# Optimization experiments

Measured on AMD Instinct MI355X. Metric: run time of the kernel, lower is better.

Reference implementation:

```python
import jax, jax.numpy as jnp
import numpy as np

C = 1.0                      # ball curvature c
SQRT_C = 1.0                 # sqrt(c)
EPS = 1e-15                  # norm clamp
BALL_EPS = 1e-5              # projection margin
B, DIN, DOUT = 262144, 128, 128


def artanh(u):
    u = jnp.clip(u, -1.0 + 1e-7, 1.0 - 1e-7)
    return 0.5 * (jnp.log1p(u) - jnp.log1p(-u))


def mobius_matvec(W, x):
    # x: [B, din], W: [dout, din]
    x_norm = jnp.clip(jnp.linalg.norm(x, axis=-1, keepdims=True), EPS)
    Mx = x @ W.T                                   # [B, dout]
    Mx_norm = jnp.clip(jnp.linalg.norm(Mx, axis=-1, keepdims=True), EPS)
    scale = jnp.tanh(Mx_norm / x_norm * artanh(SQRT_C * x_norm)) / (Mx_norm * SQRT_C)
    res = scale * Mx
    return jnp.where(Mx_norm <= 1e-10, 0.0, res)


def mobius_add(x, y):
    # x: [B, d], y broadcastable to [B, d]
    x2 = jnp.sum(x * x, axis=-1, keepdims=True)
    y2 = jnp.sum(y * y, axis=-1, keepdims=True)
    xy = jnp.sum(x * y, axis=-1, keepdims=True)
    num = (1.0 + 2.0 * C * xy + C * y2) * x + (1.0 - C * x2) * y
    den = jnp.clip(1.0 + 2.0 * C * xy + C * C * x2 * y2, EPS)
    return num / den


def projx(x):
    norm = jnp.clip(jnp.linalg.norm(x, axis=-1, keepdims=True), EPS)
    maxnorm = (1.0 - BALL_EPS) / SQRT_C
    return jnp.where(norm > maxnorm, x / norm * maxnorm, x)


def setup_inputs() -> dict:
    key = jax.random.key(0)
    k1, k2, k3 = jax.random.split(key, 3)
    # points strictly inside the unit ball: randn * 0.05 -> norm ~ 0.57 max tail-safe
    x = jax.random.normal(k1, (B, DIN), dtype=jnp.float32) * 0.05
    fan = np.sqrt(6.0 / (DIN + DOUT))  # xavier_uniform scale
    weight = jax.random.uniform(k2, (DOUT, DIN), dtype=jnp.float32, minval=-fan, maxval=fan)
    bias = jax.random.normal(k3, (DOUT,), dtype=jnp.float32) * 0.05
    return {"x": x, "weight": weight, "bias": bias}


def reference(x, weight, bias):
    y = mobius_matvec(weight, x)
    y = mobius_add(y, bias[None, :])
    return projx(y)
```

## Files before the change

kernel.cpp:

```cpp
#include <hip/hip_runtime.h>

typedef __attribute__((ext_vector_type(8))) short short8;
typedef __attribute__((ext_vector_type(4))) float floatx4;

__device__ __forceinline__ unsigned short f2b(float f) {
    union { float f; unsigned int i; } v; v.f = f;
    unsigned int u = v.i;
    u += 0x7FFFu + ((u >> 16) & 1u);
    return (unsigned short)(u >> 16);
}

__global__ __launch_bounds__(256) void mobius_linear_kernel(
    const float* __restrict__ X,
    const float* __restrict__ W,
    const float* __restrict__ Bias,
    float* __restrict__ Out)
{
    __shared__ unsigned short ldsW[128 * 136];

    const int tid  = threadIdx.x;
    const int wave = tid >> 6;
    const int lane = tid & 63;
    const int q = lane >> 4;
    const int c = lane & 15;

#pragma unroll
    for (int i = 0; i < 8; ++i) {
        int chunk = i * 256 + tid;
        int row = chunk >> 4, cc = chunk & 15;
        const float* src = W + row * 128 + cc * 8;
        floatx4 w0 = *reinterpret_cast<const floatx4*>(src);
        floatx4 w1 = *reinterpret_cast<const floatx4*>(src + 4);
        short8 pk;
#pragma unroll
        for (int j = 0; j < 4; ++j) { pk[j] = (short)f2b(w0[j]); pk[4 + j] = (short)f2b(w1[j]); }
        *reinterpret_cast<short8*>(&ldsW[row * 136 + cc * 8]) = pk;
    }

    float bias_f[8];
#pragma unroll
    for (int n = 0; n < 8; ++n) bias_f[n] = Bias[n * 16 + c];
    float b2 = 0.f;
#pragma unroll
    for (int n = 0; n < 8; ++n) b2 = fmaf(bias_f[n], bias_f[n], b2);
    b2 += __shfl_xor(b2, 1);
    b2 += __shfl_xor(b2, 2);
    b2 += __shfl_xor(b2, 4);
    b2 += __shfl_xor(b2, 8);

    const int rowbase = blockIdx.x * 128 + wave * 32;

    short8 afrag[2][4];
    float xn2[2] = {0.f, 0.f};
#pragma unroll
    for (int g = 0; g < 2; ++g) {
        const float* xrow = X + (size_t)(rowbase + g * 16 + c) * 128;
#pragma unroll
        for (int kc = 0; kc < 4; ++kc) {
            const float* src = xrow + kc * 32 + q * 8;
            floatx4 x0 = *reinterpret_cast<const floatx4*>(src);
            floatx4 x1 = *reinterpret_cast<const floatx4*>(src + 4);
            short8 pk;
#pragma unroll
            for (int j = 0; j < 4; ++j) {
                xn2[g] = fmaf(x0[j], x0[j], xn2[g]);
                xn2[g] = fmaf(x1[j], x1[j], xn2[g]);
                pk[j] = (short)f2b(x0[j]); pk[4 + j] = (short)f2b(x1[j]);
            }
            afrag[g][kc] = pk;
        }
    }
    xn2[0] += __shfl_xor(xn2[0], 16); xn2[0] += __shfl_xor(xn2[0], 32);
    xn2[1] += __shfl_xor(xn2[1], 16); xn2[1] += __shfl_xor(xn2[1], 32);

    __syncthreads();

    floatx4 acc[2][8];
#pragma unroll
    for (int g = 0; g < 2; ++g)
#pragma unroll
        for (int n = 0; n < 8; ++n)
            acc[g][n] = (floatx4){0.f, 0.f, 0.f, 0.f};

#pragma unroll
    for (int kc = 0; kc < 4; ++kc) {
#pragma unroll
        for (int n = 0; n < 8; ++n) {
            short8 bf = *reinterpret_cast<const short8*>(
                &ldsW[(n * 16 + c) * 136 + kc * 32 + q * 8]);
            acc[0][n] = __builtin_amdgcn_mfma_f32_16x16x32_bf16(afrag[0][kc], bf, acc[0][n], 0, 0, 0);
            acc[1][n] = __builtin_amdgcn_mfma_f32_16x16x32_bf16(afrag[1][kc], bf, acc[1][n], 0, 0, 0);
        }
    }

#pragma unroll
    for (int g = 0; g < 2; ++g) {
        float m2[4], mb[4];
#pragma unroll
        for (int r = 0; r < 4; ++r) {
            float s2 = 0.f, sb = 0.f;
#pragma unroll
            for (int n = 0; n < 8; ++n) {
                float v = acc[g][n][r];
                s2 = fmaf(v, v, s2);
                sb = fmaf(v, bias_f[n], sb);
            }
            m2[r] = s2; mb[r] = sb;
        }
#pragma unroll
        for (int r = 0; r < 4; ++r) {
            m2[r] += __shfl_xor(m2[r], 1); mb[r] += __shfl_xor(mb[r], 1);
            m2[r] += __shfl_xor(m2[r], 2); mb[r] += __shfl_xor(mb[r], 2);
            m2[r] += __shfl_xor(m2[r], 4); mb[r] += __shfl_xor(mb[r], 4);
            m2[r] += __shfl_xor(m2[r], 8); mb[r] += __shfl_xor(mb[r], 8);
        }
#pragma unroll
        for (int r = 0; r < 4; ++r) {
            float xr2   = __shfl(xn2[g], q * 4 + r);
            float xnorm = fmaxf(sqrtf(xr2), 1e-15f);
            float u     = fminf(xnorm, 1.f - 1e-7f);
            float at    = 0.5f * __logf((1.f + u) / (1.f - u));
            float Mxn   = fmaxf(sqrtf(m2[r]), 1e-15f);
            float arg   = Mxn / xnorm * at;
            float e     = __expf(2.f * arg);
            float th    = 1.f - 2.f / (e + 1.f);
            float scale = (Mxn <= 1e-10f) ? 0.f : th / Mxn;
            float y2 = scale * scale * m2[r];
            float yb = scale * mb[r];
            float t1  = 1.f + 2.f * yb + b2;
            float den = fmaxf(fmaf(y2, b2, 1.f + 2.f * yb), 1e-15f);
            float Af = t1 * scale / den;
            float Bf = (1.f - y2) / den;
            float zn2 = Af * Af * m2[r] + 2.f * Af * Bf * mb[r] + Bf * Bf * b2;
            float zn  = fmaxf(sqrtf(zn2), 1e-15f);
            const float maxn = 1.f - 1e-5f;
            float fac = (zn > maxn) ? (maxn / zn) : 1.f;
            Af *= fac; Bf *= fac;

            int row = rowbase + g * 16 + q * 4 + r;
            float* orow = Out + (size_t)row * 128;
#pragma unroll
            for (int n = 0; n < 8; ++n) {
                orow[n * 16 + c] = fmaf(Af, acc[g][n][r], Bf * bias_f[n]);
            }
        }
    }
}

extern "C" void kernel_launch(void* const* d_in, const int* in_sizes, int n_in,
                              void* d_out, int out_size, void* d_ws, size_t ws_size,
                              hipStream_t stream) {
    const float* X    = (const float*)d_in[0];
    const float* W    = (const float*)d_in[1];
    const float* Bias = (const float*)d_in[2];
    float* Out = (float*)d_out;

    dim3 grid(2048), block(256);
    hipLaunchKernelGGL(mobius_linear_kernel, grid, block, 0, stream, X, W, Bias, Out);
}
```

Baseline: 251.8 us.

## Pre-convert weights to bf16 in a separate kernel and drop LDS staging

Adds a small kernel that converts W to bf16 once into the workspace. The main kernel then reads B fragments straight from global memory (cached) instead of having every block convert W and stage it in LDS. It also halves rows per wave (16 instead of 32) and doubles the grid to 4096 blocks, adding a launch-bounds occupancy hint. This removes the per-block W conversion, the LDS traffic and the __syncthreads, at the cost of an extra launch, repeated global or L2 weight reads per wave, and less reuse of each weight fragment.

```diff
diff --git a/kernel.cpp b/kernel.cpp
--- a/kernel.cpp
+++ b/kernel.cpp
@@ -1,6 +1,7 @@
 #include <hip/hip_runtime.h>
 
 typedef __attribute__((ext_vector_type(8))) short short8;
+typedef __attribute__((ext_vector_type(4))) short short4v;
 typedef __attribute__((ext_vector_type(4))) float floatx4;
 
 __device__ __forceinline__ unsigned short f2b(float f) {
@@ -10,32 +11,30 @@
     return (unsigned short)(u >> 16);
 }
 
-__global__ __launch_bounds__(256) void mobius_linear_kernel(
+__global__ __launch_bounds__(256) void convert_w_kernel(
+    const float* __restrict__ W, unsigned short* __restrict__ Wb)
+{
+    int i = (blockIdx.x * 256 + threadIdx.x) * 4;
+    floatx4 w = *reinterpret_cast<const floatx4*>(W + i);
+    short4v p;
+#pragma unroll
+    for (int j = 0; j < 4; ++j) p[j] = (short)f2b(w[j]);
+    *reinterpret_cast<short4v*>(Wb + i) = p;
+}
+
+__global__ __launch_bounds__(256, 5) void mobius_linear_kernel(
     const float* __restrict__ X,
-    const float* __restrict__ W,
+    const unsigned short* __restrict__ Wb,
     const float* __restrict__ Bias,
     float* __restrict__ Out)
 {
-    __shared__ unsigned short ldsW[128 * 136];
-
     const int tid  = threadIdx.x;
     const int wave = tid >> 6;
     const int lane = tid & 63;
     const int q = lane >> 4;
     const int c = lane & 15;
 
-#pragma unroll
-    for (int i = 0; i < 8; ++i) {
-        int chunk = i * 256 + tid;
-        int row = chunk >> 4, cc = chunk & 15;
-        const float* src = W + row * 128 + cc * 8;
-        floatx4 w0 = *reinterpret_cast<const floatx4*>(src);
-        floatx4 w1 = *reinterpret_cast<const floatx4*>(src + 4);
-        short8 pk;
-#pragma unroll
-        for (int j = 0; j < 4; ++j) { pk[j] = (short)f2b(w0[j]); pk[4 + j] = (short)f2b(w1[j]); }
-        *reinterpret_cast<short8*>(&ldsW[row * 136 + cc * 8]) = pk;
-    }
+    const int rowbase = blockIdx.x * 64 + wave * 16;
 
     float bias_f[8];
 #pragma unroll
@@ -48,101 +47,87 @@
     b2 += __shfl_xor(b2, 4);
     b2 += __shfl_xor(b2, 8);
 
-    const int rowbase = blockIdx.x * 128 + wave * 32;
+    short8 afrag[4];
+    float xn2 = 0.f;
+    const float* xrow = X + (size_t)(rowbase + c) * 128;
+#pragma unroll
+    for (int kc = 0; kc < 4; ++kc) {
+        const float* src = xrow + kc * 32 + q * 8;
+        floatx4 x0 = *reinterpret_cast<const floatx4*>(src);
+        floatx4 x1 = *reinterpret_cast<const floatx4*>(src + 4);
+        short8 pk;
+#pragma unroll
+        for (int j = 0; j < 4; ++j) {
+            xn2 = fmaf(x0[j], x0[j], xn2);
+            xn2 = fmaf(x1[j], x1[j], xn2);
+            pk[j] = (short)f2b(x0[j]); pk[4 + j] = (short)f2b(x1[j]);
+        }
+        afrag[kc] = pk;
+    }
+    xn2 += __shfl_xor(xn2, 16);
+    xn2 += __shfl_xor(xn2, 32);
 
-    short8 afrag[2][4];
-    float xn2[2] = {0.f, 0.f};
+    floatx4 acc[8];
 #pragma unroll
-    for (int g = 0; g < 2; ++g) {
-        const float* xrow = X + (size_t)(rowbase + g * 16 + c) * 128;
+    for (int n = 0; n < 8; ++n) acc[n] = (floatx4){0.f, 0.f, 0.f, 0.f};
+
+#pragma unroll
+    for (int n = 0; n < 8; ++n) {
+        const unsigned short* wrow = Wb + (n * 16 + c) * 128 + q * 8;
 #pragma unroll
         for (int kc = 0; kc < 4; ++kc) {
-            const float* src = xrow + kc * 32 + q * 8;
-            floatx4 x0 = *reinterpret_cast<const floatx4*>(src);
-            floatx4 x1 = *reinterpret_cast<const floatx4*>(src + 4);
-            short8 pk;
-#pragma unroll
-            for (int j = 0; j < 4; ++j) {
-                xn2[g] = fmaf(x0[j], x0[j], xn2[g]);
-                xn2[g] = fmaf(x1[j], x1[j], xn2[g]);
-                pk[j] = (short)f2b(x0[j]); pk[4 + j] = (short)f2b(x1[j]);
-            }
-            afrag[g][kc] = pk;
-        }
-    }
-    xn2[0] += __shfl_xor(xn2[0], 16); xn2[0] += __shfl_xor(xn2[0], 32);
-    xn2[1] += __shfl_xor(xn2[1], 16); xn2[1] += __shfl_xor(xn2[1], 32);
-
-    __syncthreads();
-
-    floatx4 acc[2][8];
-#pragma unroll
-    for (int g = 0; g < 2; ++g)
-#pragma unroll
-        for (int n = 0; n < 8; ++n)
-            acc[g][n] = (floatx4){0.f, 0.f, 0.f, 0.f};
-
-#pragma unroll
-    for (int kc = 0; kc < 4; ++kc) {
-#pragma unroll
-        for (int n = 0; n < 8; ++n) {
-            short8 bf = *reinterpret_cast<const short8*>(
-                &ldsW[(n * 16 + c) * 136 + kc * 32 + q * 8]);
-            acc[0][n] = __builtin_amdgcn_mfma_f32_16x16x32_bf16(afrag[0][kc], bf, acc[0][n], 0, 0, 0);
-            acc[1][n] = __builtin_amdgcn_mfma_f32_16x16x32_bf16(afrag[1][kc], bf, acc[1][n], 0, 0, 0);
+            short8 bf = *reinterpret_cast<const short8*>(wrow + kc * 32);
+            acc[n] = __builtin_amdgcn_mfma_f32_16x16x32_bf16(afrag[kc], bf, acc[n], 0, 0, 0);
         }
     }
 
+    float m2[4], mb[4];
 #pragma unroll
-    for (int g = 0; g < 2; ++g) {
-        float m2[4], mb[4];
+    for (int r = 0; r < 4; ++r) {
+        float s2 = 0.f, sb = 0.f;
 #pragma unroll
-        for (int r = 0; r < 4; ++r) {
-            float s2 = 0.f, sb = 0.f;
+        for (int n = 0; n < 8; ++n) {
+            float v = acc[n][r];
+            s2 = fmaf(v, v, s2);
+            sb = fmaf(v, bias_f[n], sb);
+        }
+        m2[r] = s2; mb[r] = sb;
+    }
 #pragma unroll
-            for (int n = 0; n < 8; ++n) {
-                float v = acc[g][n][r];
-                s2 = fmaf(v, v, s2);
-                sb = fmaf(v, bias_f[n], sb);
-            }
-            m2[r] = s2; mb[r] = sb;
-        }
+    for (int r = 0; r < 4; ++r) {
+        m2[r] += __shfl_xor(m2[r], 1); mb[r] += __shfl_xor(mb[r], 1);
+        m2[r] += __shfl_xor(m2[r], 2); mb[r] += __shfl_xor(mb[r], 2);
+        m2[r] += __shfl_xor(m2[r], 4); mb[r] += __shfl_xor(mb[r], 4);
+        m2[r] += __shfl_xor(m2[r], 8); mb[r] += __shfl_xor(mb[r], 8);
+    }
 #pragma unroll
-        for (int r = 0; r < 4; ++r) {
-            m2[r] += __shfl_xor(m2[r], 1); mb[r] += __shfl_xor(mb[r], 1);
-            m2[r] += __shfl_xor(m2[r], 2); mb[r] += __shfl_xor(mb[r], 2);
-            m2[r] += __shfl_xor(m2[r], 4); mb[r] += __shfl_xor(mb[r], 4);
-            m2[r] += __shfl_xor(m2[r], 8); mb[r] += __shfl_xor(mb[r], 8);
-        }
+    for (int r = 0; r < 4; ++r) {
+        float xr2   = __shfl(xn2, q * 4 + r);
+        float xnorm = fmaxf(sqrtf(xr2), 1e-15f);
+        float u     = fminf(xnorm, 1.f - 1e-7f);
+        float at    = 0.5f * __logf((1.f + u) / (1.f - u));
+        float Mxn   = fmaxf(sqrtf(m2[r]), 1e-15f);
+        float arg   = Mxn / xnorm * at;
+        float e     = __expf(2.f * arg);
+        float th    = 1.f - 2.f / (e + 1.f);
+        float scale = (Mxn <= 1e-10f) ? 0.f : th / Mxn;
+        float y2 = scale * scale * m2[r];
+        float yb = scale * mb[r];
+        float t1  = 1.f + 2.f * yb + b2;
+        float den = fmaxf(fmaf(y2, b2, 1.f + 2.f * yb), 1e-15f);
+        float Af = t1 * scale / den;
+        float Bf = (1.f - y2) / den;
+        float zn2 = Af * Af * m2[r] + 2.f * Af * Bf * mb[r] + Bf * Bf * b2;
+        float zn  = fmaxf(sqrtf(zn2), 1e-15f);
+        const float maxn = 1.f - 1e-5f;
+        float fac = (zn > maxn) ? (maxn / zn) : 1.f;
+        Af *= fac; Bf *= fac;
+
+        int row = rowbase + q * 4 + r;
+        float* orow = Out + (size_t)row * 128;
 #pragma unroll
-        for (int r = 0; r < 4; ++r) {
-            float xr2   = __shfl(xn2[g], q * 4 + r);
-            float xnorm = fmaxf(sqrtf(xr2), 1e-15f);
-            float u     = fminf(xnorm, 1.f - 1e-7f);
-            float at    = 0.5f * __logf((1.f + u) / (1.f - u));
-            float Mxn   = fmaxf(sqrtf(m2[r]), 1e-15f);
-            float arg   = Mxn / xnorm * at;
-            float e     = __expf(2.f * arg);
-            float th    = 1.f - 2.f / (e + 1.f);
-            float scale = (Mxn <= 1e-10f) ? 0.f : th / Mxn;
-            float y2 = scale * scale * m2[r];
-            float yb = scale * mb[r];
-            float t1  = 1.f + 2.f * yb + b2;
-            float den = fmaxf(fmaf(y2, b2, 1.f + 2.f * yb), 1e-15f);
-            float Af = t1 * scale / den;
-            float Bf = (1.f - y2) / den;
-            float zn2 = Af * Af * m2[r] + 2.f * Af * Bf * mb[r] + Bf * Bf * b2;
-            float zn  = fmaxf(sqrtf(zn2), 1e-15f);
-            const float maxn = 1.f - 1e-5f;
-            float fac = (zn > maxn) ? (maxn / zn) : 1.f;
-            Af *= fac; Bf *= fac;
-
-            int row = rowbase + g * 16 + q * 4 + r;
-            float* orow = Out + (size_t)row * 128;
-#pragma unroll
-            for (int n = 0; n < 8; ++n) {
-                orow[n * 16 + c] = fmaf(Af, acc[g][n][r], Bf * bias_f[n]);
-            }
+        for (int n = 0; n < 8; ++n) {
+            orow[n * 16 + c] = fmaf(Af, acc[n][r], Bf * bias_f[n]);
         }
     }
 }
@@ -154,7 +139,9 @@
     const float* W    = (const float*)d_in[1];
     const float* Bias = (const float*)d_in[2];
     float* Out = (float*)d_out;
+    unsigned short* Wb = (unsigned short*)d_ws;
 
-    dim3 grid(2048), block(256);
-    hipLaunchKernelGGL(mobius_linear_kernel, grid, block, 0, stream, X, W, Bias, Out);
+    hipLaunchKernelGGL(convert_w_kernel, dim3(16), dim3(256), 0, stream, W, Wb);
+    hipLaunchKernelGGL(mobius_linear_kernel, dim3(4096), dim3(256), 0, stream,
+                       X, Wb, Bias, Out);
 }
```

After: 277.3 us. +10.1%, slower.

## Pre-convert weights to bf16, swizzle LDS, permute output columns for vector stores

Applied to the files above, without the earlier changes.

Adds a small pre-kernel that converts W to bf16 once into workspace, so each block loads half the bytes and skips per-block conversion. The LDS layout is changed from padded to XOR-style swizzled. The N-column mapping is permuted so each lane owns 8 contiguous output columns, which allows 16-byte vector stores and vector bias loads instead of scalar strided stores. X packing now uses a perm-based bf16 truncation with rounding, and launch bounds request 4 waves per SIMD. The cost is an extra kernel launch.

```diff
diff --git a/kernel.cpp b/kernel.cpp
--- a/kernel.cpp
+++ b/kernel.cpp
@@ -1,6 +1,8 @@
 #include <hip/hip_runtime.h>
 
 typedef __attribute__((ext_vector_type(8))) short short8;
+typedef __attribute__((ext_vector_type(4))) short short4v;
+typedef __attribute__((ext_vector_type(4))) int   int4v;
 typedef __attribute__((ext_vector_type(4))) float floatx4;
 
 __device__ __forceinline__ unsigned short f2b(float f) {
@@ -10,13 +12,30 @@
     return (unsigned short)(u >> 16);
 }
 
-__global__ __launch_bounds__(256) void mobius_linear_kernel(
+__device__ __forceinline__ int pack2(float f0, float f1) {
+    unsigned int u0 = __float_as_uint(f0) + 0x8000u;
+    unsigned int u1 = __float_as_uint(f1) + 0x8000u;
+    return (int)__builtin_amdgcn_perm(u1, u0, 0x07060302u);
+}
+
+__global__ __launch_bounds__(256) void convert_w_kernel(
+    const float* __restrict__ W, unsigned short* __restrict__ Wb)
+{
+    int i = (blockIdx.x * 256 + threadIdx.x) * 4;
+    floatx4 w = *reinterpret_cast<const floatx4*>(W + i);
+    short4v p;
+#pragma unroll
+    for (int j = 0; j < 4; ++j) p[j] = (short)f2b(w[j]);
+    *reinterpret_cast<short4v*>(Wb + i) = p;
+}
+
+__global__ __launch_bounds__(256, 4) void mobius_linear_kernel(
     const float* __restrict__ X,
-    const float* __restrict__ W,
+    const unsigned short* __restrict__ Wb,
     const float* __restrict__ Bias,
     float* __restrict__ Out)
 {
-    __shared__ unsigned short ldsW[128 * 136];
+    __shared__ unsigned short ldsW[128 * 128];
 
     const int tid  = threadIdx.x;
     const int wave = tid >> 6;
@@ -27,26 +46,11 @@
 #pragma unroll
     for (int i = 0; i < 8; ++i) {
         int chunk = i * 256 + tid;
-        int row = chunk >> 4, cc = chunk & 15;
-        const float* src = W + row * 128 + cc * 8;
-        floatx4 w0 = *reinterpret_cast<const floatx4*>(src);
-        floatx4 w1 = *reinterpret_cast<const floatx4*>(src + 4);
-        short8 pk;
-#pragma unroll
-        for (int j = 0; j < 4; ++j) { pk[j] = (short)f2b(w0[j]); pk[4 + j] = (short)f2b(w1[j]); }
-        *reinterpret_cast<short8*>(&ldsW[row * 136 + cc * 8]) = pk;
+        int row = chunk >> 4, j = chunk & 15;
+        short8 v = *reinterpret_cast<const short8*>(Wb + row * 128 + j * 8);
+        int s = (j + (row >> 3)) & 15;
+        *reinterpret_cast<short8*>(&ldsW[row * 128 + s * 8]) = v;
     }
-
-    float bias_f[8];
-#pragma unroll
-    for (int n = 0; n < 8; ++n) bias_f[n] = Bias[n * 16 + c];
-    float b2 = 0.f;
-#pragma unroll
-    for (int n = 0; n < 8; ++n) b2 = fmaf(bias_f[n], bias_f[n], b2);
-    b2 += __shfl_xor(b2, 1);
-    b2 += __shfl_xor(b2, 2);
-    b2 += __shfl_xor(b2, 4);
-    b2 += __shfl_xor(b2, 8);
 
     const int rowbase = blockIdx.x * 128 + wave * 32;
 
@@ -60,18 +64,33 @@
             const float* src = xrow + kc * 32 + q * 8;
             floatx4 x0 = *reinterpret_cast<const floatx4*>(src);
             floatx4 x1 = *reinterpret_cast<const floatx4*>(src + 4);
-            short8 pk;
 #pragma unroll
             for (int j = 0; j < 4; ++j) {
                 xn2[g] = fmaf(x0[j], x0[j], xn2[g]);
                 xn2[g] = fmaf(x1[j], x1[j], xn2[g]);
-                pk[j] = (short)f2b(x0[j]); pk[4 + j] = (short)f2b(x1[j]);
             }
-            afrag[g][kc] = pk;
+            int4v pk;
+            pk[0] = pack2(x0[0], x0[1]); pk[1] = pack2(x0[2], x0[3]);
+            pk[2] = pack2(x1[0], x1[1]); pk[3] = pack2(x1[2], x1[3]);
+            union { int4v i; short8 s; } u; u.i = pk;
+            afrag[g][kc] = u.s;
         }
     }
     xn2[0] += __shfl_xor(xn2[0], 16); xn2[0] += __shfl_xor(xn2[0], 32);
     xn2[1] += __shfl_xor(xn2[1], 16); xn2[1] += __shfl_xor(xn2[1], 32);
+
+    floatx4 blo = *reinterpret_cast<const floatx4*>(Bias + c * 8);
+    floatx4 bhi = *reinterpret_cast<const floatx4*>(Bias + c * 8 + 4);
+    float bias_f[8];
+#pragma unroll
+    for (int j = 0; j < 4; ++j) { bias_f[j] = blo[j]; bias_f[4 + j] = bhi[j]; }
+    float b2 = 0.f;
+#pragma unroll
+    for (int n = 0; n < 8; ++n) b2 = fmaf(bias_f[n], bias_f[n], b2);
+    b2 += __shfl_xor(b2, 1);
+    b2 += __shfl_xor(b2, 2);
+    b2 += __shfl_xor(b2, 4);
+    b2 += __shfl_xor(b2, 8);
 
     __syncthreads();
 
@@ -84,10 +103,11 @@
 
 #pragma unroll
     for (int kc = 0; kc < 4; ++kc) {
+        const int s8 = ((kc * 4 + q + c) & 15) * 8;
 #pragma unroll
         for (int n = 0; n < 8; ++n) {
             short8 bf = *reinterpret_cast<const short8*>(
-                &ldsW[(n * 16 + c) * 136 + kc * 32 + q * 8]);
+                &ldsW[(c * 8 + n) * 128 + s8]);
             acc[0][n] = __builtin_amdgcn_mfma_f32_16x16x32_bf16(afrag[0][kc], bf, acc[0][n], 0, 0, 0);
             acc[1][n] = __builtin_amdgcn_mfma_f32_16x16x32_bf16(afrag[1][kc], bf, acc[1][n], 0, 0, 0);
         }
@@ -138,11 +158,15 @@
             Af *= fac; Bf *= fac;
 
             int row = rowbase + g * 16 + q * 4 + r;
-            float* orow = Out + (size_t)row * 128;
+            float* orow = Out + (size_t)row * 128 + c * 8;
+            floatx4 lo, hi;
 #pragma unroll
-            for (int n = 0; n < 8; ++n) {
-                orow[n * 16 + c] = fmaf(Af, acc[g][n][r], Bf * bias_f[n]);
+            for (int n = 0; n < 4; ++n) {
+                lo[n] = fmaf(Af, acc[g][n][r],     Bf * bias_f[n]);
+                hi[n] = fmaf(Af, acc[g][4 + n][r], Bf * bias_f[4 + n]);
             }
+            *reinterpret_cast<floatx4*>(orow)     = lo;
+            *reinterpret_cast<floatx4*>(orow + 4) = hi;
         }
     }
 }
@@ -154,7 +178,9 @@
     const float* W    = (const float*)d_in[1];
     const float* Bias = (const float*)d_in[2];
     float* Out = (float*)d_out;
+    unsigned short* Wb = (unsigned short*)d_ws;
 
-    dim3 grid(2048), block(256);
-    hipLaunchKernelGGL(mobius_linear_kernel, grid, block, 0, stream, X, W, Bias, Out);
+    hipLaunchKernelGGL(convert_w_kernel, dim3(16), dim3(256), 0, stream, W, Wb);
+    hipLaunchKernelGGL(mobius_linear_kernel, dim3(2048), dim3(256), 0, stream,
+                       X, Wb, Bias, Out);
 }
```

Result: slower. 259.0 us (+2.9%).
